# Kernel optimization log

Measured on AMD Instinct MI355X. Metric: run time of the kernel, lower is better.

Reference implementation:

```python
import jax, jax.numpy as jnp
import numpy as np

EPS = 1e-5
D = 4  # max_displacement


def _conv(x, w, b, stride, pad):
    # x: [B,C,H,W], w: [O,I,kh,kw]
    y = jax.lax.conv_general_dilated(x, w, (stride, stride), [(pad, pad), (pad, pad)],
                                     dimension_numbers=('NCHW', 'OIHW', 'NCHW'))
    return y + b[None, :, None, None]


def _bn(x, g, b, m, v):
    # eval-mode batchnorm with running stats
    scale = (g * jax.lax.rsqrt(v + EPS))[None, :, None, None]
    return (x - m[None, :, None, None]) * scale + b[None, :, None, None]


def _extract(x, w1, b1, g1, be1, m1, v1, w2, b2, g2, be2, m2, v2, w3, b3, g3, be3, m3, v3):
    x = jax.nn.relu(_bn(_conv(x, w1, b1, 2, 3), g1, be1, m1, v1))
    x = jax.nn.relu(_bn(_conv(x, w2, b2, 2, 1), g2, be2, m2, v2))
    x = jax.nn.relu(_bn(_conv(x, w3, b3, 2, 1), g3, be3, m3, v3))
    return x  # [B,256,H/8,W/8]


def _correlation(x1, x2):
    # shifted-window correlation, 81 shifts (structural loop, static slices)
    B, C, H, W = x1.shape
    x2p = jnp.pad(x2, ((0, 0), (0, 0), (D, D), (D, D)))
    maps = [jnp.sum(x1 * x2p[:, :, i:i + H, j:j + W], axis=1)
            for i in range(2 * D + 1) for j in range(2 * D + 1)]
    return jnp.stack(maps, axis=1)  # [B,81,H,W]


def _gmm(cloth_img, person_img, fe, fw1, fb1, fw2, fb2, fw3, fb3):
    cf = _extract(cloth_img, *fe)
    pf = _extract(person_img, *fe)
    corr = _correlation(cf, pf)
    x = jax.nn.relu(_conv(corr, fw1, fb1, 1, 1))
    x = jax.nn.relu(_conv(x, fw2, fb2, 1, 1))
    return _conv(x, fw3, fb3, 1, 1)  # [B,2,H/8,W/8]


def setup_inputs() -> dict:
    key = jax.random.key(0)
    ks = jax.random.split(key, 32)
    B, H, W = 8, 512, 512
    w = lambda k, shape, s=0.05: jax.random.normal(k, shape, jnp.float32) * s
    inp = {}
    inp['cloth_img'] = jax.random.normal(ks[0], (B, 3, H, W), jnp.float32)
    inp['person_img'] = jax.random.normal(ks[1], (B, 3, H, W), jnp.float32)
    inp['w1'] = w(ks[2], (64, 3, 7, 7)); inp['b1'] = w(ks[3], (64,))
    inp['g1'] = 1.0 + w(ks[4], (64,)); inp['be1'] = w(ks[5], (64,))
    inp['m1'] = w(ks[6], (64,)); inp['v1'] = jax.random.uniform(ks[7], (64,), jnp.float32, 0.5, 1.5)
    inp['w2'] = w(ks[8], (128, 64, 3, 3)); inp['b2'] = w(ks[9], (128,))
    inp['g2'] = 1.0 + w(ks[10], (128,)); inp['be2'] = w(ks[11], (128,))
    inp['m2'] = w(ks[12], (128,)); inp['v2'] = jax.random.uniform(ks[13], (128,), jnp.float32, 0.5, 1.5)
    inp['w3'] = w(ks[14], (256, 128, 3, 3)); inp['b3'] = w(ks[15], (256,))
    inp['g3'] = 1.0 + w(ks[16], (256,)); inp['be3'] = w(ks[17], (256,))
    inp['m3'] = w(ks[18], (256,)); inp['v3'] = jax.random.uniform(ks[19], (256,), jnp.float32, 0.5, 1.5)
    inp['fw1'] = w(ks[20], (128, 81, 3, 3)); inp['fb1'] = w(ks[21], (128,))
    inp['fw2'] = w(ks[22], (64, 128, 3, 3)); inp['fb2'] = w(ks[23], (64,))
    inp['fw3'] = w(ks[24], (2, 64, 3, 3)); inp['fb3'] = w(ks[25], (2,))
    return inp


def reference(cloth_img, person_img,
              w1, b1, g1, be1, m1, v1,
              w2, b2, g2, be2, m2, v2,
              w3, b3, g3, be3, m3, v3,
              fw1, fb1, fw2, fb2, fw3, fb3):
    fe = (w1, b1, g1, be1, m1, v1, w2, b2, g2, be2, m2, v2, w3, b3, g3, be3, m3, v3)
    return _gmm(cloth_img, person_img, fe, fw1, fb1, fw2, fb2, fw3, fb3)
```

## Files before the change

### kernel.cpp

```cpp
#include <hip/hip_runtime.h>

typedef __bf16 bf16x8_t __attribute__((ext_vector_type(8)));
typedef float f32x4 __attribute__((ext_vector_type(4)));
typedef unsigned short u16x8 __attribute__((ext_vector_type(8)));
typedef unsigned short u16x4 __attribute__((ext_vector_type(4)));

#define EPS 1e-5f

__device__ __forceinline__ unsigned short f2bf(float f) {
    unsigned u = __builtin_bit_cast(unsigned, f);
    u += 0x7fff + ((u >> 16) & 1);
    return (unsigned short)(u >> 16);
}

__device__ __forceinline__ void gload16(const unsigned short* g, unsigned short* l) {
    __builtin_amdgcn_global_load_lds(
        (const __attribute__((address_space(1))) unsigned int*)g,
        (__attribute__((address_space(3))) unsigned int*)l,
        16, 0, 0);
}

template <int N> __device__ __forceinline__ void s_waitcnt_vm() {
    if constexpr (N == 0)       asm volatile("s_waitcnt vmcnt(0)" ::: "memory");
    else if constexpr (N == 4)  asm volatile("s_waitcnt vmcnt(4)" ::: "memory");
    else if constexpr (N == 6)  asm volatile("s_waitcnt vmcnt(6)" ::: "memory");
    else if constexpr (N == 8)  asm volatile("s_waitcnt vmcnt(8)" ::: "memory");
    else if constexpr (N == 10) asm volatile("s_waitcnt vmcnt(10)" ::: "memory");
    else if constexpr (N == 12) asm volatile("s_waitcnt vmcnt(12)" ::: "memory");
    else static_assert(N == 0, "unsupported vmcnt");
}

__device__ __forceinline__ void wconv3x3(const float* __restrict__ w, unsigned short* __restrict__ dst,
                                         int Cout, int Kp, int CIN, int CINP, int idx) {
    int m = idx / Kp, k = idx - m * Kp;
    int tap = k / CINP, ic = k - tap * CINP;
    unsigned short v = 0;
    if (m < Cout && tap < 9 && ic < CIN) {
        int kh = tap / 3, kw = tap - kh * 3;
        v = f2bf(w[((m * CIN + ic) * 3 + kh) * 3 + kw]);
    }
    dst[idx] = v;
}

__global__ void conv_weights_all(const float* __restrict__ w1, const float* __restrict__ w2,
                                 const float* __restrict__ w3, const float* __restrict__ fw1,
                                 const float* __restrict__ fw2, const float* __restrict__ fw3,
                                 const float* __restrict__ b1, const float* __restrict__ g1,
                                 const float* __restrict__ be1, const float* __restrict__ m1,
                                 const float* __restrict__ v1,
                                 const float* __restrict__ b2, const float* __restrict__ g2,
                                 const float* __restrict__ be2, const float* __restrict__ m2,
                                 const float* __restrict__ v2,
                                 const float* __restrict__ b3, const float* __restrict__ g3,
                                 const float* __restrict__ be3, const float* __restrict__ m3,
                                 const float* __restrict__ v3,
                                 const float* __restrict__ fb1, const float* __restrict__ fb2,
                                 const float* __restrict__ fb3,
                                 unsigned short* d1, unsigned short* d2, unsigned short* d3,
                                 unsigned short* d4, unsigned short* d5, unsigned short* d6,
                                 float* __restrict__ aff) {
    int idx = blockIdx.x * 256 + threadIdx.x;
    if (idx < 16384) {
        int m = idx >> 8, k = idx & 255;
        int kh = k >> 5, r = k & 31, kw = r >> 2, ic = r & 3;
        unsigned short v = 0;
        if (kh < 7 && kw < 7 && ic < 3) v = f2bf(w1[((m * 3 + ic) * 7 + kh) * 7 + kw]);
        d1[idx] = v;
    } else if (idx < 90112)  wconv3x3(w2, d2, 128, 576, 64, 64, idx - 16384);
    else if (idx < 385024)   wconv3x3(w3, d3, 256, 1152, 128, 128, idx - 90112);
    else if (idx < 532480)   wconv3x3(fw1, d4, 128, 1152, 81, 128, idx - 385024);
    else if (idx < 606208)   wconv3x3(fw2, d5, 64, 1152, 128, 128, idx - 532480);
    else if (idx < 643072)   wconv3x3(fw3, d6, 2, 576, 64, 64, idx - 606208);
    else {
        int i = idx - 643072;
        if (i < 64) {
            float s = g1[i] * rsqrtf(v1[i] + EPS);
            aff[i] = s; aff[64 + i] = (b1[i] - m1[i]) * s + be1[i];
        } else if (i < 192) {
            int c = i - 64; float s = g2[c] * rsqrtf(v2[c] + EPS);
            aff[128 + c] = s; aff[256 + c] = (b2[c] - m2[c]) * s + be2[c];
        } else if (i < 448) {
            int c = i - 192; float s = g3[c] * rsqrtf(v3[c] + EPS);
            aff[384 + c] = s; aff[640 + c] = (b3[c] - m3[c]) * s + be3[c];
        } else if (i < 576) {
            int c = i - 448; aff[896 + c] = 1.f; aff[1024 + c] = fb1[c];
        } else if (i < 640) {
            int c = i - 576; aff[1152 + c] = 1.f; aff[1216 + c] = fb2[c];
        } else if (i < 642) {
            int c = i - 640; aff[1280 + c] = 1.f; aff[1288 + c] = fb3[c];
        }
    }
}

__global__ void to_nhwc4(const float* __restrict__ cloth, const float* __restrict__ person,
                         unsigned short* __restrict__ dst) {
    int z = blockIdx.z;
    const float* src = (z < 8) ? cloth + (size_t)z * 786432
                               : person + (size_t)(z - 8) * 786432;
    int p = blockIdx.x * 256 + threadIdx.x;
    int row = p >> 9, col = p & 511;
    u16x4 o;
    o[0] = f2bf(src[p]);
    o[1] = f2bf(src[262144 + p]);
    o[2] = f2bf(src[524288 + p]);
    o[3] = 0;
    *(u16x4*)&dst[(size_t)z * 1073296 + ((size_t)(row + 3) * 518 + col + 3) * 4] = o;
}

__device__ __forceinline__ void ring1_zero(unsigned short* __restrict__ buf, int Hp, int Wp,
                                           int C8, int imgStrideElems, int nimg, int idx) {
    int nb = 2 * Wp + 2 * (Hp - 2);
    int per = nb * C8;
    if (idx >= per * nimg) return;
    int z = idx / per, q = idx - z * per;
    int p = q / C8, cc = q - p * C8;
    int row, col;
    if (p < Wp) { row = 0; col = p; }
    else if (p < 2 * Wp) { row = Hp - 1; col = p - Wp; }
    else { int e = p - 2 * Wp; row = 1 + (e >> 1); col = (e & 1) ? Wp - 1 : 0; }
    const u16x8 zv = {0, 0, 0, 0, 0, 0, 0, 0};
    *(u16x8*)&buf[(size_t)z * imgStrideElems + ((size_t)row * Wp + col) * (C8 * 8) + cc * 8] = zv;
}

__global__ void zero_pads(unsigned short* __restrict__ nhwc, unsigned short* __restrict__ t1,
                          unsigned short* __restrict__ t2, unsigned short* __restrict__ corr,
                          unsigned short* __restrict__ f1b, unsigned short* __restrict__ f2b) {
    int idx = blockIdx.x * 256 + threadIdx.x;
    if (blockIdx.y == 0) {
        if (idx >= 16 * 6180) return;
        int z = idx / 6180, p = idx - z * 6180;
        int r, c;
        if (p < 1554) { r = p / 518; c = p - (p / 518) * 518; }
        else if (p < 3108) { int q = p - 1554; r = 515 + q / 518; c = q - (q / 518) * 518; }
        else { int q = p - 3108; r = 3 + q / 6; int k = q - (q / 6) * 6; c = (k < 3) ? k : 512 + k; }
        const u16x4 zv = {0, 0, 0, 0};
        *(u16x4*)&nhwc[(size_t)z * 1073296 + ((size_t)r * 518 + c) * 4] = zv;
    } else if (blockIdx.y == 1) {
        ring1_zero(t1, 258, 258, 8, 4260096, 16, idx);
    } else if (blockIdx.y == 2) {
        ring1_zero(t2, 130, 130, 16, 2163200, 16, idx);
    } else {
        if (idx < 33280) ring1_zero(corr, 66, 66, 16, 557568, 8, idx);
        else if (idx < 66560) ring1_zero(f1b, 66, 66, 16, 557568, 8, idx - 33280);
        else if (idx < 83200) ring1_zero(f2b, 66, 66, 8, 278784, 8, idx - 66560);
    }
}

template <int WR, int WS, int MODE, bool RELU, bool OUT_NCHW, int CIN, int NKT,
          int HIN, int WOS, int STRIDE, int OPAD, int PIPE>
__global__ __launch_bounds__(WR * WS * 64)
void gemm_conv(const unsigned short* __restrict__ X, const unsigned short* __restrict__ Wmk,
               const float* __restrict__ scale, const float* __restrict__ shift,
               void* __restrict__ Yv, int Cout, int xImgStride, int yImgStride) {
    constexpr int BR = WR * 64, BS = WS * 64, NT = WR * WS * 64;
    constexpr int SXC = BR * 8 / NT, SWC = BS * 8 / NT;
    constexpr int NLOAD = SXC + SWC;
    constexpr int KP = (MODE == 1) ? NKT * 64 : 256;
    constexpr int WP = HIN + ((MODE == 2) ? 6 : 2);
    constexpr int WOUT = 1 << WOS;
    constexpr int WOP = WOUT + 2 * OPAD;
    constexpr int NBUF = PIPE ? 2 : 1;
    constexpr int EPS_LDK = BS + 8;
    constexpr int GEMM_ELEMS = NBUF * (BR + BS) * 64;
    constexpr int EPI_ELEMS = BR * EPS_LDK;
    constexpr int LDS_ELEMS = GEMM_ELEMS > EPI_ELEMS ? GEMM_ELEMS : EPI_ELEMS;
    __shared__ __align__(16) unsigned short lds[LDS_ELEMS];
    unsigned short* XsB = lds;
    unsigned short* WsB = lds + NBUF * BR * 64;
    const int tid = threadIdx.x;
    const int lane = tid & 63, wid = tid >> 6;
    const int wr = wid % WR, wsx = wid / WR;
    int bx = blockIdx.x;
    { const int nx = gridDim.x; bx = (bx & 7) * (nx >> 3) + (bx >> 3); }
    const int r0 = bx * BR, s0 = blockIdx.y * BS;
    const int z = blockIdx.z;
    const int lr = lane & 15, lk = lane >> 4;
    const unsigned short* Ximg = X + (size_t)z * xImgStride;

    const unsigned short* xsrc[SXC];
    #pragma unroll
    for (int i = 0; i < SXC; ++i) {
        int c = i * NT + tid;
        int row = c >> 3, chs = (c & 7) ^ (row & 7);
        int r = r0 + row;
        int oh = r >> WOS, ow = r & (WOUT - 1);
        if (MODE == 1)
            xsrc[i] = Ximg + ((size_t)(oh * STRIDE) * WP + (size_t)(ow * STRIDE)) * CIN + chs * 8;
        else
            xsrc[i] = Ximg + ((size_t)(2 * oh + (chs >> 2)) * WP + 2 * ow + (chs & 3) * 2) * 4;
    }
    const unsigned short* wsrc[SWC];
    #pragma unroll
    for (int i = 0; i < SWC; ++i) {
        int c = i * NT + tid;
        int row = c >> 3, chs = (c & 7) ^ (row & 7);
        wsrc[i] = Wmk + (size_t)(s0 + row) * KP + chs * 8;
    }

    int arow[4], brow[4];
    #pragma unroll
    for (int mi = 0; mi < 4; ++mi) arow[mi] = (wr * 64 + mi * 16 + lr) * 64;
    #pragma unroll
    for (int si = 0; si < 4; ++si) brow[si] = (wsx * 64 + si * 16 + lr) * 64;

    const f32x4 fz = {0.f, 0.f, 0.f, 0.f};
    f32x4 acc[4][4];
    #pragma unroll
    for (int a = 0; a < 4; ++a)
        #pragma unroll
        for (int b = 0; b < 4; ++b) acc[a][b] = fz;

    auto stage = [&](int kt, int b) {
        size_t koff;
        if (MODE == 1) {
            const int tap = (kt * 64) / CIN;
            const int kh = tap / 3, kw = tap - (tap / 3) * 3;
            const int icb0 = (kt * 64) % CIN;
            koff = ((size_t)kh * WP + kw) * CIN + icb0;
        } else {
            koff = (size_t)kt * 2 * WP * 4;
        }
        #pragma unroll
        for (int i = 0; i < SXC; ++i)
            gload16(xsrc[i] + koff, &XsB[b * BR * 64 + (i * NT + wid * 64) * 8]);
        #pragma unroll
        for (int i = 0; i < SWC; ++i)
            gload16(wsrc[i] + (size_t)kt * 64, &WsB[b * BS * 64 + (i * NT + wid * 64) * 8]);
    };
    auto compute = [&](int b) {
        #pragma unroll
        for (int hf = 0; hf < 2; ++hf) {
            const int cA = (((hf * 4 + lk) ^ (lr & 7)) * 8);
            u16x8 af[4], bfr[4];
            #pragma unroll
            for (int mi = 0; mi < 4; ++mi) af[mi] = *(const u16x8*)&XsB[b * BR * 64 + arow[mi] + cA];
            #pragma unroll
            for (int si = 0; si < 4; ++si) bfr[si] = *(const u16x8*)&WsB[b * BS * 64 + brow[si] + cA];
            #pragma unroll
            for (int mi = 0; mi < 4; ++mi)
                #pragma unroll
                for (int si = 0; si < 4; ++si)
                    acc[mi][si] = __builtin_amdgcn_mfma_f32_16x16x32_bf16(
                        __builtin_bit_cast(bf16x8_t, af[mi]),
                        __builtin_bit_cast(bf16x8_t, bfr[si]), acc[mi][si], 0, 0, 0);
        }
    };

    if (PIPE == 0) {
        #pragma unroll
        for (int kt = 0; kt < NKT; ++kt) {
            stage(kt, 0);
            __syncthreads();
            compute(0);
            __syncthreads();
        }
    } else {
        stage(0, 0);
        #pragma unroll
        for (int kt = 0; kt < NKT; ++kt) {
            const int cur = kt & 1;
            if (kt + 1 < NKT) {
                stage(kt + 1, cur ^ 1);
                s_waitcnt_vm<NLOAD>();
            } else {
                s_waitcnt_vm<0>();
            }
            __builtin_amdgcn_sched_barrier(0);
            __builtin_amdgcn_s_barrier();
            __builtin_amdgcn_sched_barrier(0);
            compute(cur);
            __builtin_amdgcn_sched_barrier(0);
            __builtin_amdgcn_s_barrier();
        }
    }

    if (OUT_NCHW) {
        #pragma unroll
        for (int si = 0; si < 4; ++si) {
            int col = s0 + wsx * 64 + si * 16 + lr;
            bool cok = col < Cout;
            float sc = cok ? scale[col] : 0.f;
            float sh = cok ? shift[col] : 0.f;
            #pragma unroll
            for (int mi = 0; mi < 4; ++mi) {
                int rbase = r0 + wr * 64 + mi * 16 + lk * 4;
                #pragma unroll
                for (int j = 0; j < 4; ++j) {
                    float v = acc[mi][si][j] * sc + sh;
                    if (RELU) v = fmaxf(v, 0.f);
                    if (cok) ((float*)Yv)[(size_t)z * yImgStride + col * 4096 + rbase + j] = v;
                }
            }
        }
    } else {
        __syncthreads();
        unsigned short* epi = lds;
        #pragma unroll
        for (int si = 0; si < 4; ++si) {
            int col = wsx * 64 + si * 16 + lr;
            float sc = scale[s0 + col];
            float sh = shift[s0 + col];
            #pragma unroll
            for (int mi = 0; mi < 4; ++mi) {
                int rowl = wr * 64 + mi * 16 + lk * 4;
                #pragma unroll
                for (int j = 0; j < 4; ++j) {
                    float v = acc[mi][si][j] * sc + sh;
                    if (RELU) v = fmaxf(v, 0.f);
                    epi[(rowl + j) * EPS_LDK + col] = f2bf(v);
                }
            }
        }
        __syncthreads();
        constexpr int NCH = BR * BS / 8 / NT;
        constexpr int CPR = BS / 8;
        #pragma unroll
        for (int i = 0; i < NCH; ++i) {
            int c = i * NT + tid;
            int row = c / CPR, colc = c - (c / CPR) * CPR;
            int r = r0 + row;
            int oh = r >> WOS, ow = r & (WOUT - 1);
            size_t off = ((size_t)(oh + OPAD) * WOP + ow + OPAD) * Cout + s0 + colc * 8;
            *(u16x8*)((unsigned short*)Yv + (size_t)z * yImgStride + off) =
                *(const u16x8*)&epi[row * EPS_LDK + colc * 8];
        }
    }
}

__global__ __launch_bounds__(256)
void corr_mfma(const unsigned short* __restrict__ cf,
               const unsigned short* __restrict__ pf,
               unsigned short* __restrict__ out) {
    const int h = blockIdx.x;
    const int di = (int)blockIdx.y - 4;
    const int z = blockIdx.z;
    const int tid = threadIdx.x;
    const int lane = tid & 63, t = tid >> 6;
    const int lr = lane & 15, lk = lane >> 4;
    const unsigned short* cfi = cf + (size_t)z * 1048576;
    const unsigned short* pfi = pf + (size_t)z * 1048576;
    unsigned short* outp = out + (size_t)z * 557568;

    u16x8 a[8];
    {
        const unsigned short* ap = cfi + ((size_t)(h * 64 + t * 16 + lr)) * 256 + lk * 8;
        #pragma unroll
        for (int ks = 0; ks < 8; ++ks) a[ks] = *(const u16x8*)(ap + ks * 32);
    }

    const u16x8 zz = {0, 0, 0, 0, 0, 0, 0, 0};
    const int h2 = h + di;
    const bool hok = (unsigned)h2 < 64u;
    #pragma unroll
    for (int ct = 0; ct < 2; ++ct) {
        const int wpg = t * 16 - 8 + ct * 16 + lr;
        u16x8 b[8];
        if (hok && (unsigned)wpg < 64u) {
            const unsigned short* bp = pfi + ((size_t)(h2 * 64 + wpg)) * 256 + lk * 8;
            #pragma unroll
            for (int ks = 0; ks < 8; ++ks) b[ks] = *(const u16x8*)(bp + ks * 32);
        } else {
            #pragma unroll
            for (int ks = 0; ks < 8; ++ks) b[ks] = zz;
        }
        f32x4 acc0 = {0.f, 0.f, 0.f, 0.f}, acc1 = {0.f, 0.f, 0.f, 0.f};
        #pragma unroll
        for (int ks = 0; ks < 8; ks += 2) {
            acc0 = __builtin_amdgcn_mfma_f32_16x16x32_bf16(
                __builtin_bit_cast(bf16x8_t, a[ks]),
                __builtin_bit_cast(bf16x8_t, b[ks]), acc0, 0, 0, 0);
            acc1 = __builtin_amdgcn_mfma_f32_16x16x32_bf16(
                __builtin_bit_cast(bf16x8_t, a[ks + 1]),
                __builtin_bit_cast(bf16x8_t, b[ks + 1]), acc1, 0, 0, 0);
        }
        const int wl = lk * 4;
        const int wpl = ct * 16 - 8 + lr;
        #pragma unroll
        for (int j = 0; j < 4; ++j) {
            int dj = wpl - (wl + j);
            if (dj >= -4 && dj <= 4) {
                int s = (di + 4) * 9 + dj + 4;
                int w = t * 16 + wl + j;
                outp[((size_t)(h + 1) * 66 + w + 1) * 128 + s] =
                    f2bf(acc0[j] + acc1[j]);
            }
        }
    }
}

extern "C" void kernel_launch(void* const* d_in, const int* in_sizes, int n_in,
                              void* d_out, int out_size, void* d_ws, size_t ws_size,
                              hipStream_t stream) {
    const float* cloth  = (const float*)d_in[0];
    const float* person = (const float*)d_in[1];
    const float* w1 = (const float*)d_in[2];  const float* b1 = (const float*)d_in[3];
    const float* g1 = (const float*)d_in[4];  const float* be1 = (const float*)d_in[5];
    const float* m1 = (const float*)d_in[6];  const float* v1 = (const float*)d_in[7];
    const float* w2 = (const float*)d_in[8];  const float* b2 = (const float*)d_in[9];
    const float* g2 = (const float*)d_in[10]; const float* be2 = (const float*)d_in[11];
    const float* m2 = (const float*)d_in[12]; const float* v2 = (const float*)d_in[13];
    const float* w3 = (const float*)d_in[14]; const float* b3 = (const float*)d_in[15];
    const float* g3 = (const float*)d_in[16]; const float* be3 = (const float*)d_in[17];
    const float* m3 = (const float*)d_in[18]; const float* v3 = (const float*)d_in[19];
    const float* fw1 = (const float*)d_in[20]; const float* fb1 = (const float*)d_in[21];
    const float* fw2 = (const float*)d_in[22]; const float* fb2 = (const float*)d_in[23];
    const float* fw3 = (const float*)d_in[24]; const float* fb3 = (const float*)d_in[25];

    char* ws = (char*)d_ws;
    auto U = [&](size_t off) { return (unsigned short*)(ws + off); };
    unsigned short* nhwc = U(0);
    unsigned short* t1   = U(34345472);
    unsigned short* cf   = U(34345472);
    unsigned short* t2   = U(170668544);
    unsigned short* w1mk  = U(239890944);
    unsigned short* w2mk  = U(239923712);
    unsigned short* w3mk  = U(240071168);
    unsigned short* fw1mk = U(240660992);
    unsigned short* fw2mk = U(240955904);
    unsigned short* fw3mk = U(241103360);
    float* aff = (float*)(ws + 241177088);
    unsigned short* corr = U(241185280);
    unsigned short* f1b  = U(250106368);
    unsigned short* f2b  = U(259027456);
    float *s1 = aff,         *sh1 = aff + 64,   *s2 = aff + 128,  *sh2 = aff + 256;
    float *s3 = aff + 384,   *sh3 = aff + 640,  *sf1 = aff + 896, *shf1 = aff + 1024;
    float *sf2 = aff + 1152, *shf2 = aff + 1216, *sf3 = aff + 1280, *shf3 = aff + 1288;

    conv_weights_all<<<2516, 256, 0, stream>>>(w1, w2, w3, fw1, fw2, fw3,
                                               b1, g1, be1, m1, v1, b2, g2, be2, m2, v2,
                                               b3, g3, be3, m3, v3, fb1, fb2, fb3,
                                               w1mk, w2mk, w3mk, fw1mk, fw2mk, fw3mk, aff);

    zero_pads<<<dim3(516, 4), 256, 0, stream>>>(nhwc, t1, t2, corr, f1b, f2b);

    to_nhwc4<<<dim3(1024, 1, 16), 256, 0, stream>>>(cloth, person, nhwc);

    gemm_conv<4, 1, 2, true, false, 4, 4, 512, 8, 2, 1, 0><<<dim3(256, 1, 16), 256, 0, stream>>>(
        nhwc, w1mk, s1, sh1, t1, 64, 1073296, 4260096);
    gemm_conv<4, 2, 1, true, false, 64, 9, 256, 7, 2, 1, 1><<<dim3(64, 1, 16), 512, 0, stream>>>(
        t1, w2mk, s2, sh2, t2, 128, 4260096, 2163200);
    gemm_conv<4, 2, 1, true, false, 128, 18, 128, 6, 2, 0, 1><<<dim3(16, 2, 16), 512, 0, stream>>>(
        t2, w3mk, s3, sh3, cf, 256, 2163200, 1048576);

    corr_mfma<<<dim3(64, 9, 8), 256, 0, stream>>>(cf, cf + (size_t)8 * 1048576, corr);

    gemm_conv<2, 2, 1, true, false, 128, 18, 64, 6, 1, 1, 1><<<dim3(32, 1, 8), 256, 0, stream>>>(
        corr, fw1mk, sf1, shf1, f1b, 128, 557568, 557568);
    gemm_conv<2, 1, 1, true, false, 128, 18, 64, 6, 1, 1, 1><<<dim3(32, 1, 8), 128, 0, stream>>>(
        f1b, fw2mk, sf2, shf2, f2b, 64, 557568, 278784);
    gemm_conv<2, 1, 1, false, true, 64, 9, 64, 6, 1, 0, 1><<<dim3(32, 1, 8), 128, 0, stream>>>(
        f2b, fw3mk, sf3, shf3, (float*)d_out, 2, 278784, 8192);
}
```

Measured before the change: 278.7 us.

## Merge prep kernels into one launch and shrink conv tile sizes for more blocks

Combines the weight conversion, padding-ring zeroing and NHWC input conversion into a single prep kernel, which removes two launches and their gaps. It also shrinks the WR tile parameter for conv2, conv3 and the first flow conv, which halves block sizes and doubles grid sizes to put more blocks on the CUs. Smaller tiles reuse less weight and activation data per block, and one larger grid mixes differently shaped work. Nothing orders the zeroing against the interior writes, but they touch disjoint regions.

```diff
diff --git a/kernel.cpp b/kernel.cpp
--- a/kernel.cpp
+++ b/kernel.cpp
@@ -40,71 +40,6 @@
         v = f2bf(w[((m * CIN + ic) * 3 + kh) * 3 + kw]);
     }
     dst[idx] = v;
-}
-
-__global__ void conv_weights_all(const float* __restrict__ w1, const float* __restrict__ w2,
-                                 const float* __restrict__ w3, const float* __restrict__ fw1,
-                                 const float* __restrict__ fw2, const float* __restrict__ fw3,
-                                 const float* __restrict__ b1, const float* __restrict__ g1,
-                                 const float* __restrict__ be1, const float* __restrict__ m1,
-                                 const float* __restrict__ v1,
-                                 const float* __restrict__ b2, const float* __restrict__ g2,
-                                 const float* __restrict__ be2, const float* __restrict__ m2,
-                                 const float* __restrict__ v2,
-                                 const float* __restrict__ b3, const float* __restrict__ g3,
-                                 const float* __restrict__ be3, const float* __restrict__ m3,
-                                 const float* __restrict__ v3,
-                                 const float* __restrict__ fb1, const float* __restrict__ fb2,
-                                 const float* __restrict__ fb3,
-                                 unsigned short* d1, unsigned short* d2, unsigned short* d3,
-                                 unsigned short* d4, unsigned short* d5, unsigned short* d6,
-                                 float* __restrict__ aff) {
-    int idx = blockIdx.x * 256 + threadIdx.x;
-    if (idx < 16384) {
-        int m = idx >> 8, k = idx & 255;
-        int kh = k >> 5, r = k & 31, kw = r >> 2, ic = r & 3;
-        unsigned short v = 0;
-        if (kh < 7 && kw < 7 && ic < 3) v = f2bf(w1[((m * 3 + ic) * 7 + kh) * 7 + kw]);
-        d1[idx] = v;
-    } else if (idx < 90112)  wconv3x3(w2, d2, 128, 576, 64, 64, idx - 16384);
-    else if (idx < 385024)   wconv3x3(w3, d3, 256, 1152, 128, 128, idx - 90112);
-    else if (idx < 532480)   wconv3x3(fw1, d4, 128, 1152, 81, 128, idx - 385024);
-    else if (idx < 606208)   wconv3x3(fw2, d5, 64, 1152, 128, 128, idx - 532480);
-    else if (idx < 643072)   wconv3x3(fw3, d6, 2, 576, 64, 64, idx - 606208);
-    else {
-        int i = idx - 643072;
-        if (i < 64) {
-            float s = g1[i] * rsqrtf(v1[i] + EPS);
-            aff[i] = s; aff[64 + i] = (b1[i] - m1[i]) * s + be1[i];
-        } else if (i < 192) {
-            int c = i - 64; float s = g2[c] * rsqrtf(v2[c] + EPS);
-            aff[128 + c] = s; aff[256 + c] = (b2[c] - m2[c]) * s + be2[c];
-        } else if (i < 448) {
-            int c = i - 192; float s = g3[c] * rsqrtf(v3[c] + EPS);
-            aff[384 + c] = s; aff[640 + c] = (b3[c] - m3[c]) * s + be3[c];
-        } else if (i < 576) {
-            int c = i - 448; aff[896 + c] = 1.f; aff[1024 + c] = fb1[c];
-        } else if (i < 640) {
-            int c = i - 576; aff[1152 + c] = 1.f; aff[1216 + c] = fb2[c];
-        } else if (i < 642) {
-            int c = i - 640; aff[1280 + c] = 1.f; aff[1288 + c] = fb3[c];
-        }
-    }
-}
-
-__global__ void to_nhwc4(const float* __restrict__ cloth, const float* __restrict__ person,
-                         unsigned short* __restrict__ dst) {
-    int z = blockIdx.z;
-    const float* src = (z < 8) ? cloth + (size_t)z * 786432
-                               : person + (size_t)(z - 8) * 786432;
-    int p = blockIdx.x * 256 + threadIdx.x;
-    int row = p >> 9, col = p & 511;
-    u16x4 o;
-    o[0] = f2bf(src[p]);
-    o[1] = f2bf(src[262144 + p]);
-    o[2] = f2bf(src[524288 + p]);
-    o[3] = 0;
-    *(u16x4*)&dst[(size_t)z * 1073296 + ((size_t)(row + 3) * 518 + col + 3) * 4] = o;
 }
 
 __device__ __forceinline__ void ring1_zero(unsigned short* __restrict__ buf, int Hp, int Wp,
@@ -122,27 +57,94 @@
     *(u16x8*)&buf[(size_t)z * imgStrideElems + ((size_t)row * Wp + col) * (C8 * 8) + cc * 8] = zv;
 }
 
-__global__ void zero_pads(unsigned short* __restrict__ nhwc, unsigned short* __restrict__ t1,
-                          unsigned short* __restrict__ t2, unsigned short* __restrict__ corr,
-                          unsigned short* __restrict__ f1b, unsigned short* __restrict__ f2b) {
-    int idx = blockIdx.x * 256 + threadIdx.x;
-    if (blockIdx.y == 0) {
-        if (idx >= 16 * 6180) return;
-        int z = idx / 6180, p = idx - z * 6180;
-        int r, c;
-        if (p < 1554) { r = p / 518; c = p - (p / 518) * 518; }
-        else if (p < 3108) { int q = p - 1554; r = 515 + q / 518; c = q - (q / 518) * 518; }
-        else { int q = p - 3108; r = 3 + q / 6; int k = q - (q / 6) * 6; c = (k < 3) ? k : 512 + k; }
-        const u16x4 zv = {0, 0, 0, 0};
-        *(u16x4*)&nhwc[(size_t)z * 1073296 + ((size_t)r * 518 + c) * 4] = zv;
-    } else if (blockIdx.y == 1) {
-        ring1_zero(t1, 258, 258, 8, 4260096, 16, idx);
-    } else if (blockIdx.y == 2) {
-        ring1_zero(t2, 130, 130, 16, 2163200, 16, idx);
+__global__ void prep_all(const float* __restrict__ cloth, const float* __restrict__ person,
+                         const float* __restrict__ w1, const float* __restrict__ w2,
+                         const float* __restrict__ w3, const float* __restrict__ fw1,
+                         const float* __restrict__ fw2, const float* __restrict__ fw3,
+                         const float* __restrict__ b1, const float* __restrict__ g1,
+                         const float* __restrict__ be1, const float* __restrict__ m1,
+                         const float* __restrict__ v1,
+                         const float* __restrict__ b2, const float* __restrict__ g2,
+                         const float* __restrict__ be2, const float* __restrict__ m2,
+                         const float* __restrict__ v2,
+                         const float* __restrict__ b3, const float* __restrict__ g3,
+                         const float* __restrict__ be3, const float* __restrict__ m3,
+                         const float* __restrict__ v3,
+                         const float* __restrict__ fb1, const float* __restrict__ fb2,
+                         const float* __restrict__ fb3,
+                         unsigned short* nhwc, unsigned short* t1, unsigned short* t2,
+                         unsigned short* corr, unsigned short* f1b, unsigned short* f2b,
+                         unsigned short* d1, unsigned short* d2, unsigned short* d3,
+                         unsigned short* d4, unsigned short* d5, unsigned short* d6,
+                         float* __restrict__ aff) {
+    int b = blockIdx.x;
+    int tid = threadIdx.x;
+    if (b < 16384) {
+        int z = b >> 10;
+        const float* src = (z < 8) ? cloth + (size_t)z * 786432
+                                   : person + (size_t)(z - 8) * 786432;
+        int p = (b & 1023) * 256 + tid;
+        int row = p >> 9, col = p & 511;
+        u16x4 o;
+        o[0] = f2bf(src[p]);
+        o[1] = f2bf(src[262144 + p]);
+        o[2] = f2bf(src[524288 + p]);
+        o[3] = 0;
+        *(u16x4*)&nhwc[(size_t)z * 1073296 + ((size_t)(row + 3) * 518 + col + 3) * 4] = o;
+    } else if (b < 18900) {
+        int idx = (b - 16384) * 256 + tid;
+        if (idx < 16384) {
+            int m = idx >> 8, k = idx & 255;
+            int kh = k >> 5, r = k & 31, kw = r >> 2, ic = r & 3;
+            unsigned short v = 0;
+            if (kh < 7 && kw < 7 && ic < 3) v = f2bf(w1[((m * 3 + ic) * 7 + kh) * 7 + kw]);
+            d1[idx] = v;
+        } else if (idx < 90112)  wconv3x3(w2, d2, 128, 576, 64, 64, idx - 16384);
+        else if (idx < 385024)   wconv3x3(w3, d3, 256, 1152, 128, 128, idx - 90112);
+        else if (idx < 532480)   wconv3x3(fw1, d4, 128, 1152, 81, 128, idx - 385024);
+        else if (idx < 606208)   wconv3x3(fw2, d5, 64, 1152, 128, 128, idx - 532480);
+        else if (idx < 643072)   wconv3x3(fw3, d6, 2, 576, 64, 64, idx - 606208);
+        else {
+            int i = idx - 643072;
+            if (i < 64) {
+                float s = g1[i] * rsqrtf(v1[i] + EPS);
+                aff[i] = s; aff[64 + i] = (b1[i] - m1[i]) * s + be1[i];
+            } else if (i < 192) {
+                int c = i - 64; float s = g2[c] * rsqrtf(v2[c] + EPS);
+                aff[128 + c] = s; aff[256 + c] = (b2[c] - m2[c]) * s + be2[c];
+            } else if (i < 448) {
+                int c = i - 192; float s = g3[c] * rsqrtf(v3[c] + EPS);
+                aff[384 + c] = s; aff[640 + c] = (b3[c] - m3[c]) * s + be3[c];
+            } else if (i < 576) {
+                int c = i - 448; aff[896 + c] = 1.f; aff[1024 + c] = fb1[c];
+            } else if (i < 640) {
+                int c = i - 576; aff[1152 + c] = 1.f; aff[1216 + c] = fb2[c];
+            } else if (i < 642) {
+                int c = i - 640; aff[1280 + c] = 1.f; aff[1288 + c] = fb3[c];
+            }
+        }
     } else {
-        if (idx < 33280) ring1_zero(corr, 66, 66, 16, 557568, 8, idx);
-        else if (idx < 66560) ring1_zero(f1b, 66, 66, 16, 557568, 8, idx - 33280);
-        else if (idx < 83200) ring1_zero(f2b, 66, 66, 8, 278784, 8, idx - 66560);
+        int bb = b - 18900;
+        int role = bb / 516;
+        int idx = (bb - role * 516) * 256 + tid;
+        if (role == 0) {
+            if (idx >= 16 * 6180) return;
+            int z = idx / 6180, p = idx - z * 6180;
+            int r, c;
+            if (p < 1554) { r = p / 518; c = p - (p / 518) * 518; }
+            else if (p < 3108) { int q = p - 1554; r = 515 + q / 518; c = q - (q / 518) * 518; }
+            else { int q = p - 3108; r = 3 + q / 6; int k = q - (q / 6) * 6; c = (k < 3) ? k : 512 + k; }
+            const u16x4 zv = {0, 0, 0, 0};
+            *(u16x4*)&nhwc[(size_t)z * 1073296 + ((size_t)r * 518 + c) * 4] = zv;
+        } else if (role == 1) {
+            ring1_zero(t1, 258, 258, 8, 4260096, 16, idx);
+        } else if (role == 2) {
+            ring1_zero(t2, 130, 130, 16, 2163200, 16, idx);
+        } else {
+            if (idx < 33280) ring1_zero(corr, 66, 66, 16, 557568, 8, idx);
+            else if (idx < 66560) ring1_zero(f1b, 66, 66, 16, 557568, 8, idx - 33280);
+            else if (idx < 83200) ring1_zero(f2b, 66, 66, 8, 278784, 8, idx - 66560);
+        }
     }
 }
 
@@ -426,25 +428,22 @@
     float *s3 = aff + 384,   *sh3 = aff + 640,  *sf1 = aff + 896, *shf1 = aff + 1024;
     float *sf2 = aff + 1152, *shf2 = aff + 1216, *sf3 = aff + 1280, *shf3 = aff + 1288;
 
-    conv_weights_all<<<2516, 256, 0, stream>>>(w1, w2, w3, fw1, fw2, fw3,
-                                               b1, g1, be1, m1, v1, b2, g2, be2, m2, v2,
-                                               b3, g3, be3, m3, v3, fb1, fb2, fb3,
-                                               w1mk, w2mk, w3mk, fw1mk, fw2mk, fw3mk, aff);
-
-    zero_pads<<<dim3(516, 4), 256, 0, stream>>>(nhwc, t1, t2, corr, f1b, f2b);
-
-    to_nhwc4<<<dim3(1024, 1, 16), 256, 0, stream>>>(cloth, person, nhwc);
+    prep_all<<<20964, 256, 0, stream>>>(cloth, person, w1, w2, w3, fw1, fw2, fw3,
+                                        b1, g1, be1, m1, v1, b2, g2, be2, m2, v2,
+                                        b3, g3, be3, m3, v3, fb1, fb2, fb3,
+                                        nhwc, t1, t2, corr, f1b, f2b,
+                                        w1mk, w2mk, w3mk, fw1mk, fw2mk, fw3mk, aff);
 
     gemm_conv<4, 1, 2, true, false, 4, 4, 512, 8, 2, 1, 0><<<dim3(256, 1, 16), 256, 0, stream>>>(
         nhwc, w1mk, s1, sh1, t1, 64, 1073296, 4260096);
-    gemm_conv<4, 2, 1, true, false, 64, 9, 256, 7, 2, 1, 1><<<dim3(64, 1, 16), 512, 0, stream>>>(
+    gemm_conv<2, 2, 1, true, false, 64, 9, 256, 7, 2, 1, 1><<<dim3(128, 1, 16), 256, 0, stream>>>(
         t1, w2mk, s2, sh2, t2, 128, 4260096, 2163200);
-    gemm_conv<4, 2, 1, true, false, 128, 18, 128, 6, 2, 0, 1><<<dim3(16, 2, 16), 512, 0, stream>>>(
+    gemm_conv<2, 2, 1, true, false, 128, 18, 128, 6, 2, 0, 1><<<dim3(32, 2, 16), 256, 0, stream>>>(
         t2, w3mk, s3, sh3, cf, 256, 2163200, 1048576);
 
     corr_mfma<<<dim3(64, 9, 8), 256, 0, stream>>>(cf, cf + (size_t)8 * 1048576, corr);
 
-    gemm_conv<2, 2, 1, true, false, 128, 18, 64, 6, 1, 1, 1><<<dim3(32, 1, 8), 256, 0, stream>>>(
+    gemm_conv<1, 2, 1, true, false, 128, 18, 64, 6, 1, 1, 1><<<dim3(64, 1, 8), 128, 0, stream>>>(
         corr, fw1mk, sf1, shf1, f1b, 128, 557568, 557568);
     gemm_conv<2, 1, 1, true, false, 128, 18, 64, 6, 1, 1, 1><<<dim3(32, 1, 8), 128, 0, stream>>>(
         f1b, fw2mk, sf2, shf2, f2b, 64, 557568, 278784);
```

After: 261.4 us. 6.2% less time.
